# Optimization experiments

Hardware: AMD Instinct MI355X
Metric: run time of the kernel (lower is better)

Reference implementation:

```python
import jax, jax.numpy as jnp
import numpy as np

HIDDEN = 2048
N_HEADS = 16
HEAD_DIM = HIDDEN // N_HEADS
INV_NORM = 1.0 / float(np.sqrt(HEAD_DIM))
BETA = 1.0


def setup_inputs() -> dict:
    key = jax.random.key(0)
    ks = jax.random.split(key, 12)
    B, S, H = 2, 2048, HIDDEN
    scale = 1.0 / float(np.sqrt(H))
    return {
        "hidden_states": jax.random.normal(ks[0], (B, S, H), jnp.float32),
        "residual": jax.random.normal(ks[1], (B, S, H), jnp.float32),
        "alibi": jax.random.normal(ks[2], (B * N_HEADS, 1, S), jnp.float32),
        "Wq": jax.random.normal(ks[3], (H, H), jnp.float32) * scale,
        "bq": jnp.zeros((H,), jnp.float32),
        "Wk": jax.random.normal(ks[4], (H, H), jnp.float32) * scale,
        "bk": jnp.zeros((H,), jnp.float32),
        "Wv": jax.random.normal(ks[5], (H, H), jnp.float32) * scale,
        "bv": jnp.zeros((H,), jnp.float32),
        "Wd": jax.random.normal(ks[6], (H, H), jnp.float32) * scale,
        "bd": jnp.zeros((H,), jnp.float32),
    }


def reference(hidden_states, residual, alibi, Wq, bq, Wk, bk, Wv, bv, Wd, bd):
    B, S, H = hidden_states.shape
    # separate QKV projections (nn.Linear: x @ W^T + b)
    q = hidden_states @ Wq.T + bq
    k = hidden_states @ Wk.T + bk
    v = hidden_states @ Wv.T + bv
    # [B, n_heads, S, head_dim]
    q = q.reshape(B, S, N_HEADS, HEAD_DIM).transpose(0, 2, 1, 3)
    k = k.reshape(B, S, N_HEADS, HEAD_DIM).transpose(0, 2, 1, 3)
    v = v.reshape(B, S, N_HEADS, HEAD_DIM).transpose(0, 2, 1, 3)
    # baddbmm: scores = beta * alibi + inv_norm * q @ k^T, per (batch*head)
    alibi_bh = alibi.reshape(B, N_HEADS, 1, S)  # broadcasts over query dim
    scores = BETA * alibi_bh + INV_NORM * jnp.einsum("bhqd,bhkd->bhqk", q, k)
    probs = jax.nn.softmax(scores.astype(jnp.float32), axis=-1).astype(v.dtype)
    # attention dropout: p=0.0 (identity)
    ctx = jnp.einsum("bhqk,bhkd->bhqd", probs, v)  # [B,H,S,D]
    ctx = ctx.transpose(0, 2, 1, 3).reshape(B, S, H)
    out = ctx @ Wd.T + bd
    # hidden dropout p=0.0 then residual add (dropout_add)
    return out + residual
```

## Files before the change

### kernel.cpp

```cpp
#include <hip/hip_runtime.h>

#define HID   2048
#define NHEAD 16
#define HD    128
#define SEQ   2048
#define BATCH 2
#define MROWS (BATCH*SEQ)
#define NQKV  (3*HID)
#define INV_NORM 0.08838834764831845f
#define LOG2E    1.4426950408889634f
#define SCALE_L2 (INV_NORM*LOG2E)

typedef __attribute__((ext_vector_type(8))) __bf16 bf16x8;
typedef __attribute__((ext_vector_type(4))) float  f32x4;

typedef __attribute__((address_space(1))) void GV;
typedef __attribute__((address_space(3))) void LV;

__device__ __forceinline__ void async16(const void* g, void* l) {
  __builtin_amdgcn_global_load_lds((const GV*)g, (LV*)l, 16, 0, 0);
}

__device__ __forceinline__ unsigned short f2bf(float f) {
  unsigned u = __builtin_bit_cast(unsigned, f);
  u += 0x7FFFu + ((u >> 16) & 1u);
  return (unsigned short)(u >> 16);
}

__device__ __forceinline__ void mfma16(f32x4& c, bf16x8 a, bf16x8 b) {
  c = __builtin_amdgcn_mfma_f32_16x16x32_bf16(a, b, c, 0, 0, 0);
}

__global__ __launch_bounds__(256) void cvt_kernel(const float* __restrict__ src,
                                                  unsigned short* __restrict__ dst, int n) {
  int i = (blockIdx.x * 256 + threadIdx.x) * 4;
  if (i >= n) return;
  float4 v = *(const float4*)(src + i);
  ushort4 o;
  o.x = f2bf(v.x); o.y = f2bf(v.y); o.z = f2bf(v.z); o.w = f2bf(v.w);
  *(ushort4*)(dst + i) = o;
}

__global__ __launch_bounds__(256) void cvtw_kernel(const float* __restrict__ W0,
                                                   const float* __restrict__ W1,
                                                   const float* __restrict__ W2,
                                                   const float* __restrict__ W3,
                                                   unsigned short* __restrict__ dst) {
  int sel = blockIdx.y;
  const float* src = (sel == 0) ? W0 : (sel == 1) ? W1 : (sel == 2) ? W2 : W3;
  unsigned short* d = dst + (size_t)sel * HID * HID;
  int i = (blockIdx.x * 256 + threadIdx.x) * 4;
  float4 v = *(const float4*)(src + i);
  ushort4 o;
  o.x = f2bf(v.x); o.y = f2bf(v.y); o.z = f2bf(v.z); o.w = f2bf(v.w);
  *(ushort4*)(d + i) = o;
}

__device__ __forceinline__ void gemm_core(const unsigned short* __restrict__ A,
                                          const unsigned short* __restrict__ Bm,
                                          int K, int m0, int n0,
                                          unsigned short* As, unsigned short* Bs,
                                          f32x4 (&acc)[4][4]) {
  const int tid  = threadIdx.x;
  const int w    = tid >> 6;
  const int lane = tid & 63;
  const int l16  = lane & 15;
  const int quad = lane >> 4;
  const int wm   = (w & 1) * 64;
  const int wn   = (w >> 1) * 64;

  const f32x4 zero = {0.f, 0.f, 0.f, 0.f};
#pragma unroll
  for (int i = 0; i < 4; ++i)
#pragma unroll
    for (int j = 0; j < 4; ++j) acc[i][j] = zero;

  for (int k0 = 0; k0 < K; k0 += 64) {
    __syncthreads();
#pragma unroll
    for (int i = 0; i < 4; ++i) {
      int slot = i * 256 + w * 64 + lane;
      int r = slot >> 3;
      int c = (slot & 7) ^ (r & 7);
      async16(A  + (size_t)(m0 + r) * K + k0 + c * 8, (char*)As + (size_t)(i * 256 + w * 64) * 16);
      async16(Bm + (size_t)(n0 + r) * K + k0 + c * 8, (char*)Bs + (size_t)(i * 256 + w * 64) * 16);
    }
    __syncthreads();

#pragma unroll
    for (int kk = 0; kk < 2; ++kk) {
      bf16x8 af[4], bfp[4];
#pragma unroll
      for (int i = 0; i < 4; ++i) {
        int rr = wm + i * 16 + l16;
        af[i] = *(const bf16x8*)(As + ((rr * 8 + (((kk * 4 + quad)) ^ (rr & 7))) * 8));
      }
#pragma unroll
      for (int j = 0; j < 4; ++j) {
        int rr = wn + j * 16 + l16;
        bfp[j] = *(const bf16x8*)(Bs + ((rr * 8 + (((kk * 4 + quad)) ^ (rr & 7))) * 8));
      }
#pragma unroll
      for (int i = 0; i < 4; ++i)
#pragma unroll
        for (int j = 0; j < 4; ++j) mfma16(acc[i][j], af[i], bfp[j]);
    }
  }
}

__global__ __launch_bounds__(256) void gemm_qkv_kernel(
    const unsigned short* __restrict__ Xb, const unsigned short* __restrict__ Wb,
    const float* __restrict__ bq, const float* __restrict__ bk,
    const float* __restrict__ bv, unsigned short* __restrict__ Cout) {
  __shared__ __align__(16) unsigned short As[128 * 64];
  __shared__ __align__(16) unsigned short Bs[128 * 64];
  f32x4 acc[4][4];
  const int m0 = blockIdx.y * 128, n0 = blockIdx.x * 128;
  gemm_core(Xb, Wb, HID, m0, n0, As, Bs, acc);

  const int tid = threadIdx.x, w = tid >> 6, lane = tid & 63;
  const int l16 = lane & 15, quad = lane >> 4;
  const int wm = (w & 1) * 64, wn = (w >> 1) * 64;
#pragma unroll
  for (int j = 0; j < 4; ++j) {
    int ng = n0 + wn + j * 16 + l16;
    float bias = (ng < HID) ? bq[ng] : (ng < 2 * HID ? bk[ng - HID] : bv[ng - 2 * HID]);
#pragma unroll
    for (int i = 0; i < 4; ++i)
#pragma unroll
      for (int r = 0; r < 4; ++r) {
        int mg = m0 + wm + i * 16 + quad * 4 + r;
        Cout[(size_t)mg * NQKV + ng] = f2bf(acc[i][j][r] + bias);
      }
  }
}

__global__ __launch_bounds__(256) void gemm_out_kernel(
    const unsigned short* __restrict__ Ctx, const unsigned short* __restrict__ Wdb,
    const float* __restrict__ bd, const float* __restrict__ Res,
    float* __restrict__ Out) {
  __shared__ __align__(16) unsigned short As[128 * 64];
  __shared__ __align__(16) unsigned short Bs[128 * 64];
  f32x4 acc[4][4];
  const int m0 = blockIdx.y * 128, n0 = blockIdx.x * 128;
  gemm_core(Ctx, Wdb, HID, m0, n0, As, Bs, acc);

  const int tid = threadIdx.x, w = tid >> 6, lane = tid & 63;
  const int l16 = lane & 15, quad = lane >> 4;
  const int wm = (w & 1) * 64, wn = (w >> 1) * 64;
#pragma unroll
  for (int j = 0; j < 4; ++j) {
    int ng = n0 + wn + j * 16 + l16;
    float bias = bd[ng];
#pragma unroll
    for (int i = 0; i < 4; ++i)
#pragma unroll
      for (int r = 0; r < 4; ++r) {
        int mg = m0 + wm + i * 16 + quad * 4 + r;
        size_t off = (size_t)mg * HID + ng;
        Out[off] = acc[i][j][r] + bias + Res[off];
      }
  }
}

__global__ __launch_bounds__(256) void vtrans_kernel(const unsigned short* __restrict__ QKV,
                                                     unsigned short* __restrict__ Vt) {
  __shared__ __align__(16) unsigned short T[64][72];
  const int s0 = blockIdx.x * 64, d0 = blockIdx.y * 64, bh = blockIdx.z;
  const int b = bh >> 4, h = bh & 15;
  const int tid = threadIdx.x;
#pragma unroll
  for (int i = 0; i < 2; ++i) {
    int idx = i * 256 + tid;
    int r = idx >> 3, ch = idx & 7;
    const unsigned short* g = QKV + ((size_t)b * SEQ + s0 + r) * NQKV + 2 * HID + h * HD + d0 + ch * 8;
    *(uint4*)(&T[r][ch * 8]) = *(const uint4*)g;
  }
  __syncthreads();
#pragma unroll
  for (int i = 0; i < 2; ++i) {
    int idx = i * 256 + tid;
    int d = idx >> 3, ch = idx & 7;
    unsigned short v[8];
#pragma unroll
    for (int x = 0; x < 8; ++x) v[x] = T[ch * 8 + x][d];
    unsigned short* g = Vt + ((size_t)bh * HD + d0 + d) * SEQ + s0 + ch * 8;
    *(uint4*)g = *(const uint4*)v;
  }
}

__global__ __launch_bounds__(256) void attn_kernel(
    const unsigned short* __restrict__ QKV, const unsigned short* __restrict__ Vt,
    const float* __restrict__ alibi, unsigned short* __restrict__ Ctx) {
  __shared__ __align__(16) unsigned short Qs[64 * 128];
  __shared__ __align__(16) unsigned short Ks[64 * 128];
  __shared__ __align__(16) unsigned short Vts[128 * 64];
  __shared__ __align__(16) unsigned short Ps[64 * 72];

  const int tid = threadIdx.x, w = tid >> 6, lane = tid & 63;
  const int l16 = lane & 15, quad = lane >> 4;
  const int q0 = blockIdx.x * 64;
  const int bh = blockIdx.y, b = bh >> 4, h = bh & 15;
  const size_t rowbase = (size_t)b * SEQ;
  const float* ali = alibi + (size_t)bh * SEQ;
  const unsigned short* Vbh = Vt + (size_t)bh * HD * SEQ;

  {
    const unsigned short* qbase = QKV + (rowbase + q0) * NQKV + h * HD;
#pragma unroll
    for (int i = 0; i < 4; ++i) {
      int slot = i * 256 + w * 64 + lane;
      int r = slot >> 4, g = (slot & 15) ^ (r & 15);
      async16(qbase + (size_t)r * NQKV + g * 8, (char*)Qs + (i * 256 + w * 64) * 16);
    }
  }

  f32x4 oacc[8];
  float l_acc[4];
  const f32x4 zero = {0.f, 0.f, 0.f, 0.f};
#pragma unroll
  for (int n = 0; n < 8; ++n) oacc[n] = zero;
#pragma unroll
  for (int r = 0; r < 4; ++r) l_acc[r] = 0.f;

  for (int kt = 0; kt < SEQ / 64; ++kt) {
    __syncthreads();
    {
      const unsigned short* kbase = QKV + (rowbase + kt * 64) * NQKV + HID + h * HD;
#pragma unroll
      for (int i = 0; i < 4; ++i) {
        int slot = i * 256 + w * 64 + lane;
        int r = slot >> 4, g = (slot & 15) ^ (r & 15);
        async16(kbase + (size_t)r * NQKV + g * 8, (char*)Ks + (i * 256 + w * 64) * 16);
      }
      const unsigned short* vbase = Vbh + kt * 64;
#pragma unroll
      for (int i = 0; i < 4; ++i) {
        int slot = i * 256 + w * 64 + lane;
        int r = slot >> 3, g = (slot & 7) ^ (r & 7);
        async16(vbase + (size_t)r * SEQ + g * 8, (char*)Vts + (i * 256 + w * 64) * 16);
      }
    }
    __syncthreads();

    f32x4 sacc[4];
#pragma unroll
    for (int j = 0; j < 4; ++j) sacc[j] = zero;
#pragma unroll
    for (int ks = 0; ks < 4; ++ks) {
      int xr = (ks * 4 + quad) ^ l16;
      bf16x8 aq = *(const bf16x8*)(Qs + ((w * 16 + l16) * 16 + xr) * 8);
#pragma unroll
      for (int j = 0; j < 4; ++j) {
        bf16x8 bk = *(const bf16x8*)(Ks + ((j * 16 + l16) * 16 + xr) * 8);
        mfma16(sacc[j], aq, bk);
      }
    }

    const float* alik = ali + kt * 64;
#pragma unroll
    for (int j = 0; j < 4; ++j) {
      float aj2 = alik[j * 16 + l16] * LOG2E;
#pragma unroll
      for (int r = 0; r < 4; ++r) {
        float p = __builtin_amdgcn_exp2f(sacc[j][r] * SCALE_L2 + aj2);
        Ps[(w * 16 + quad * 4 + r) * 72 + j * 16 + l16] = f2bf(p);
        l_acc[r] += p;
      }
    }

#pragma unroll
    for (int ks = 0; ks < 2; ++ks) {
      bf16x8 ap = *(const bf16x8*)(Ps + (w * 16 + l16) * 72 + ks * 32 + quad * 8);
#pragma unroll
      for (int n = 0; n < 8; ++n) {
        int xr = (ks * 4 + quad) ^ (l16 & 7);
        bf16x8 bv = *(const bf16x8*)(Vts + ((n * 16 + l16) * 8 + xr) * 8);
        mfma16(oacc[n], ap, bv);
      }
    }
  }

  float inv[4];
#pragma unroll
  for (int r = 0; r < 4; ++r) {
    float v = l_acc[r];
#pragma unroll
    for (int off = 1; off <= 8; off <<= 1) v += __shfl_xor(v, off, 64);
    inv[r] = 1.0f / v;
  }

#pragma unroll
  for (int n = 0; n < 8; ++n)
#pragma unroll
    for (int r = 0; r < 4; ++r) {
      size_t row = rowbase + q0 + w * 16 + quad * 4 + r;
      Ctx[row * HID + h * HD + n * 16 + l16] = f2bf(oacc[n][r] * inv[r]);
    }
}

extern "C" void kernel_launch(void* const* d_in, const int* in_sizes, int n_in,
                              void* d_out, int out_size, void* d_ws, size_t ws_size,
                              hipStream_t stream) {
  const float* hidden   = (const float*)d_in[0];
  const float* residual = (const float*)d_in[1];
  const float* alibi    = (const float*)d_in[2];
  const float* Wq = (const float*)d_in[3];
  const float* bq = (const float*)d_in[4];
  const float* Wk = (const float*)d_in[5];
  const float* bk = (const float*)d_in[6];
  const float* Wv = (const float*)d_in[7];
  const float* bv = (const float*)d_in[8];
  const float* Wd = (const float*)d_in[9];
  const float* bd = (const float*)d_in[10];
  float* out = (float*)d_out;

  unsigned short* Xb    = (unsigned short*)d_ws;
  unsigned short* Wqkvb = Xb + (size_t)MROWS * HID;
  unsigned short* Wdb   = Wqkvb + (size_t)NQKV * HID;
  unsigned short* QKVb  = Wdb + (size_t)HID * HID;
  unsigned short* Ctxb  = QKVb + (size_t)MROWS * NQKV;
  unsigned short* Vtb   = Wqkvb;

  const int nX = MROWS * HID, nW = HID * HID;
  cvt_kernel<<<nX / 4 / 256, 256, 0, stream>>>(hidden, Xb, nX);
  cvtw_kernel<<<dim3(nW / 4 / 256, 4), 256, 0, stream>>>(Wq, Wk, Wv, Wd, Wqkvb);

  gemm_qkv_kernel<<<dim3(NQKV / 128, MROWS / 128), 256, 0, stream>>>(Xb, Wqkvb, bq, bk, bv, QKVb);
  vtrans_kernel<<<dim3(SEQ / 64, HD / 64, BATCH * NHEAD), 256, 0, stream>>>(QKVb, Vtb);
  attn_kernel<<<dim3(SEQ / 64, BATCH * NHEAD), 256, 0, stream>>>(QKVb, Vtb, alibi, Ctxb);
  gemm_out_kernel<<<dim3(HID / 128, MROWS / 128), 256, 0, stream>>>(Ctxb, Wdb, bd, residual, out);
}
```

Before: 488.7 us.

## Restructure attention to 128-row query tiles with 32x32x16 MFMA and register-held Q

The attention kernel now processes 128 query rows per block, with each wave owning 32 rows. Q fragments are loaded once into registers instead of being reread from LDS on every key tile. The QK^T and PV products switch from 16x16x32 to 32x32x16 bf16 MFMA, and probabilities are packed into bf16 pairs with vectorised alibi loads and LDS stores. Shared memory is aliased so Q staging reuses the K buffer, and launch bounds request two blocks per CU. The aim is to halve K/V tile loads per query and cut LDS traffic, at the cost of higher register pressure and half as many blocks.

```diff
diff --git a/kernel.cpp b/kernel.cpp
--- a/kernel.cpp
+++ b/kernel.cpp
@@ -11,8 +11,9 @@
 #define LOG2E    1.4426950408889634f
 #define SCALE_L2 (INV_NORM*LOG2E)
 
-typedef __attribute__((ext_vector_type(8))) __bf16 bf16x8;
-typedef __attribute__((ext_vector_type(4))) float  f32x4;
+typedef __attribute__((ext_vector_type(8)))  __bf16 bf16x8;
+typedef __attribute__((ext_vector_type(4)))  float  f32x4;
+typedef __attribute__((ext_vector_type(16))) float  f32x16;
 
 typedef __attribute__((address_space(1))) void GV;
 typedef __attribute__((address_space(3))) void LV;
@@ -25,6 +26,16 @@
   unsigned u = __builtin_bit_cast(unsigned, f);
   u += 0x7FFFu + ((u >> 16) & 1u);
   return (unsigned short)(u >> 16);
+}
+
+__device__ __forceinline__ unsigned pkbf(float a, float b) {
+#if __has_builtin(__builtin_amdgcn_cvt_pk_bf16_f32)
+  typedef __attribute__((ext_vector_type(2))) __bf16 bf16x2;
+  bf16x2 r = __builtin_amdgcn_cvt_pk_bf16_f32(a, b);
+  return __builtin_bit_cast(unsigned, r);
+#else
+  return (unsigned)f2bf(a) | ((unsigned)f2bf(b) << 16);
+#endif
 }
 
 __device__ __forceinline__ void mfma16(f32x4& c, bf16x8 a, bf16x8 b) {
@@ -189,113 +200,133 @@
   }
 }
 
-__global__ __launch_bounds__(256) void attn_kernel(
+__global__ __launch_bounds__(256, 2) void attn_kernel(
     const unsigned short* __restrict__ QKV, const unsigned short* __restrict__ Vt,
     const float* __restrict__ alibi, unsigned short* __restrict__ Ctx) {
-  __shared__ __align__(16) unsigned short Qs[64 * 128];
-  __shared__ __align__(16) unsigned short Ks[64 * 128];
-  __shared__ __align__(16) unsigned short Vts[128 * 64];
-  __shared__ __align__(16) unsigned short Ps[64 * 72];
+  __shared__ __align__(16) char smem[51200];
+  unsigned short* Ks  = (unsigned short*)smem;
+  unsigned short* Vts = (unsigned short*)(smem + 16384);
+  unsigned short* Ps  = (unsigned short*)(smem + 32768);
+  unsigned short* Qs  = (unsigned short*)smem;
 
   const int tid = threadIdx.x, w = tid >> 6, lane = tid & 63;
-  const int l16 = lane & 15, quad = lane >> 4;
-  const int q0 = blockIdx.x * 64;
-  const int bh = blockIdx.y, b = bh >> 4, h = bh & 15;
+  const int l32 = lane & 31, h = lane >> 5;
+  const int q0 = blockIdx.x * 128;
+  const int bh = blockIdx.y, b = bh >> 4, hh = bh & 15;
   const size_t rowbase = (size_t)b * SEQ;
   const float* ali = alibi + (size_t)bh * SEQ;
   const unsigned short* Vbh = Vt + (size_t)bh * HD * SEQ;
 
   {
-    const unsigned short* qbase = QKV + (rowbase + q0) * NQKV + h * HD;
-#pragma unroll
-    for (int i = 0; i < 4; ++i) {
+    const unsigned short* qbase = QKV + (rowbase + q0) * NQKV + hh * HD;
+#pragma unroll
+    for (int i = 0; i < 8; ++i) {
       int slot = i * 256 + w * 64 + lane;
-      int r = slot >> 4, g = (slot & 15) ^ (r & 15);
-      async16(qbase + (size_t)r * NQKV + g * 8, (char*)Qs + (i * 256 + w * 64) * 16);
-    }
-  }
-
-  f32x4 oacc[8];
-  float l_acc[4];
-  const f32x4 zero = {0.f, 0.f, 0.f, 0.f};
-#pragma unroll
-  for (int n = 0; n < 8; ++n) oacc[n] = zero;
-#pragma unroll
-  for (int r = 0; r < 4; ++r) l_acc[r] = 0.f;
+      int r = slot >> 4, c = (slot & 15) ^ (r & 15);
+      async16(qbase + (size_t)r * NQKV + c * 8, (char*)Qs + (size_t)(i * 256 + w * 64) * 16);
+    }
+  }
+  __syncthreads();
+  bf16x8 qf[8];
+  {
+    int qr = w * 32 + l32;
+#pragma unroll
+    for (int ks = 0; ks < 8; ++ks) {
+      int c = (ks * 2 + h) ^ (qr & 15);
+      qf[ks] = *(const bf16x8*)(Qs + (qr * 16 + c) * 8);
+    }
+  }
+
+  f32x16 oacc[4];
+  float l_acc = 0.f;
+#pragma unroll
+  for (int nb = 0; nb < 4; ++nb)
+#pragma unroll
+    for (int r = 0; r < 16; ++r) oacc[nb][r] = 0.f;
+
+  __syncthreads();
 
   for (int kt = 0; kt < SEQ / 64; ++kt) {
-    __syncthreads();
     {
-      const unsigned short* kbase = QKV + (rowbase + kt * 64) * NQKV + HID + h * HD;
+      const unsigned short* kbase = QKV + (rowbase + kt * 64) * NQKV + HID + hh * HD;
 #pragma unroll
       for (int i = 0; i < 4; ++i) {
         int slot = i * 256 + w * 64 + lane;
-        int r = slot >> 4, g = (slot & 15) ^ (r & 15);
-        async16(kbase + (size_t)r * NQKV + g * 8, (char*)Ks + (i * 256 + w * 64) * 16);
+        int r = slot >> 4, c = (slot & 15) ^ (r & 15);
+        async16(kbase + (size_t)r * NQKV + c * 8, (char*)Ks + (size_t)(i * 256 + w * 64) * 16);
       }
       const unsigned short* vbase = Vbh + kt * 64;
 #pragma unroll
       for (int i = 0; i < 4; ++i) {
         int slot = i * 256 + w * 64 + lane;
-        int r = slot >> 3, g = (slot & 7) ^ (r & 7);
-        async16(vbase + (size_t)r * SEQ + g * 8, (char*)Vts + (i * 256 + w * 64) * 16);
+        int r = slot >> 3, c = (slot & 7) ^ (r & 7);
+        async16(vbase + (size_t)r * SEQ + c * 8, (char*)Vts + (size_t)(i * 256 + w * 64) * 16);
       }
     }
     __syncthreads();
 
-    f32x4 sacc[4];
-#pragma unroll
-    for (int j = 0; j < 4; ++j) sacc[j] = zero;
-#pragma unroll
-    for (int ks = 0; ks < 4; ++ks) {
-      int xr = (ks * 4 + quad) ^ l16;
-      bf16x8 aq = *(const bf16x8*)(Qs + ((w * 16 + l16) * 16 + xr) * 8);
-#pragma unroll
-      for (int j = 0; j < 4; ++j) {
-        bf16x8 bk = *(const bf16x8*)(Ks + ((j * 16 + l16) * 16 + xr) * 8);
-        mfma16(sacc[j], aq, bk);
-      }
-    }
-
-    const float* alik = ali + kt * 64;
-#pragma unroll
-    for (int j = 0; j < 4; ++j) {
-      float aj2 = alik[j * 16 + l16] * LOG2E;
-#pragma unroll
-      for (int r = 0; r < 4; ++r) {
-        float p = __builtin_amdgcn_exp2f(sacc[j][r] * SCALE_L2 + aj2);
-        Ps[(w * 16 + quad * 4 + r) * 72 + j * 16 + l16] = f2bf(p);
-        l_acc[r] += p;
-      }
-    }
-
-#pragma unroll
-    for (int ks = 0; ks < 2; ++ks) {
-      bf16x8 ap = *(const bf16x8*)(Ps + (w * 16 + l16) * 72 + ks * 32 + quad * 8);
-#pragma unroll
-      for (int n = 0; n < 8; ++n) {
-        int xr = (ks * 4 + quad) ^ (l16 & 7);
-        bf16x8 bv = *(const bf16x8*)(Vts + ((n * 16 + l16) * 8 + xr) * 8);
-        mfma16(oacc[n], ap, bv);
-      }
-    }
-  }
-
-  float inv[4];
-#pragma unroll
-  for (int r = 0; r < 4; ++r) {
-    float v = l_acc[r];
-#pragma unroll
-    for (int off = 1; off <= 8; off <<= 1) v += __shfl_xor(v, off, 64);
-    inv[r] = 1.0f / v;
-  }
-
-#pragma unroll
-  for (int n = 0; n < 8; ++n)
-#pragma unroll
-    for (int r = 0; r < 4; ++r) {
-      size_t row = rowbase + q0 + w * 16 + quad * 4 + r;
-      Ctx[row * HID + h * HD + n * 16 + l16] = f2bf(oacc[n][r] * inv[r]);
+    f32x16 sacc[2];
+#pragma unroll
+    for (int mb = 0; mb < 2; ++mb)
+#pragma unroll
+      for (int r = 0; r < 16; ++r) sacc[mb][r] = 0.f;
+#pragma unroll
+    for (int ks = 0; ks < 8; ++ks) {
+      int c = (ks * 2 + h) ^ (l32 & 15);
+#pragma unroll
+      for (int mb = 0; mb < 2; ++mb) {
+        bf16x8 kf = *(const bf16x8*)(Ks + ((mb * 32 + l32) * 16 + ((ks * 2 + h) ^ (l32 & 15))) * 8);
+        sacc[mb] = __builtin_amdgcn_mfma_f32_32x32x16_bf16(kf, qf[ks], sacc[mb], 0, 0, 0);
+      }
+      (void)c;
+    }
+
+    const float* alik = ali + kt * 64 + 4 * h;
+    const int qrow = w * 32 + l32;
+#pragma unroll
+    for (int mb = 0; mb < 2; ++mb) {
+#pragma unroll
+      for (int g = 0; g < 4; ++g) {
+        float4 av = *(const float4*)(alik + mb * 32 + g * 8);
+        float p0 = __builtin_amdgcn_exp2f(sacc[mb][g * 4 + 0] * SCALE_L2 + av.x * LOG2E);
+        float p1 = __builtin_amdgcn_exp2f(sacc[mb][g * 4 + 1] * SCALE_L2 + av.y * LOG2E);
+        float p2 = __builtin_amdgcn_exp2f(sacc[mb][g * 4 + 2] * SCALE_L2 + av.z * LOG2E);
+        float p3 = __builtin_amdgcn_exp2f(sacc[mb][g * 4 + 3] * SCALE_L2 + av.w * LOG2E);
+        l_acc += (p0 + p1) + (p2 + p3);
+        uint2 pk;
+        pk.x = pkbf(p0, p1);
+        pk.y = pkbf(p2, p3);
+        *(uint2*)(Ps + qrow * 72 + mb * 32 + g * 8 + 4 * h) = pk;
+      }
+    }
+
+#pragma unroll
+    for (int ks2 = 0; ks2 < 4; ++ks2) {
+      bf16x8 pf = *(const bf16x8*)(Ps + qrow * 72 + ks2 * 16 + h * 8);
+#pragma unroll
+      for (int nb = 0; nb < 4; ++nb) {
+        bf16x8 vf = *(const bf16x8*)(Vts + ((nb * 32 + l32) * 8 + ((ks2 * 2 + h) ^ (l32 & 7))) * 8);
+        oacc[nb] = __builtin_amdgcn_mfma_f32_32x32x16_bf16(pf, vf, oacc[nb], 0, 0, 0);
+      }
+    }
+    __syncthreads();
+  }
+
+  float lf = l_acc + __shfl_xor(l_acc, 32, 64);
+  float rinv[16];
+#pragma unroll
+  for (int reg = 0; reg < 16; ++reg) {
+    int row = (reg & 3) + 8 * (reg >> 2) + 4 * h;
+    rinv[reg] = 1.0f / __shfl(lf, row, 64);
+  }
+
+#pragma unroll
+  for (int nb = 0; nb < 4; ++nb)
+#pragma unroll
+    for (int reg = 0; reg < 16; ++reg) {
+      int row = (reg & 3) + 8 * (reg >> 2) + 4 * h;
+      size_t qg = rowbase + q0 + w * 32 + row;
+      Ctx[qg * HID + hh * HD + nb * 32 + l32] = f2bf(oacc[nb][reg] * rinv[reg]);
     }
 }
 
@@ -328,6 +359,6 @@
 
   gemm_qkv_kernel<<<dim3(NQKV / 128, MROWS / 128), 256, 0, stream>>>(Xb, Wqkvb, bq, bk, bv, QKVb);
   vtrans_kernel<<<dim3(SEQ / 64, HD / 64, BATCH * NHEAD), 256, 0, stream>>>(QKVb, Vtb);
-  attn_kernel<<<dim3(SEQ / 64, BATCH * NHEAD), 256, 0, stream>>>(QKVb, Vtb, alibi, Ctxb);
+  attn_kernel<<<dim3(SEQ / 128, BATCH * NHEAD), 256, 0, stream>>>(QKVb, Vtb, alibi, Ctxb);
   gemm_out_kernel<<<dim3(HID / 128, MROWS / 128), 256, 0, stream>>>(Ctxb, Wdb, bd, residual, out);
 }
```

After: 440.9 us. 1.11x faster.
